# Kernel tuning notes

Hardware: AMD Instinct MI355X
Metric: run time of the kernel (lower is better)

Reference implementation:

```python
import jax, jax.numpy as jnp
import numpy as np

NEG_SLOPE = 0.2
BN_EPS = 1e-5


def _gat(x, src, dst, W, a_src, a_dst, b, concat):
    """PyG GATConv (eval mode, self-loops already in src/dst)."""
    N = x.shape[0]
    H, C = a_src.shape
    h = (x @ W).reshape(N, H, C)                      # [N,H,C]
    s = (h * a_src).sum(-1)                           # [N,H] per-node src score
    d = (h * a_dst).sum(-1)                           # [N,H] per-node dst score
    e = jax.nn.leaky_relu(s[src] + d[dst], NEG_SLOPE)  # [E,H]
    m = jax.ops.segment_max(e, dst, num_segments=N)   # segment softmax over dst
    ex = jnp.exp(e - m[dst])
    denom = jax.ops.segment_sum(ex, dst, num_segments=N)
    alpha = ex / denom[dst]                           # [E,H]
    out = jax.ops.segment_sum(alpha[:, :, None] * h[src], dst, num_segments=N)  # [N,H,C]
    out = out.reshape(N, H * C) if concat else out.mean(axis=1)
    return out + b


def _bn(x, g, beta, rm, rv):
    return (x - rm) * (g / jnp.sqrt(rv + BN_EPS)) + beta


def setup_inputs() -> dict:
    key = jax.random.key(0)
    ks = jax.random.split(key, 32)
    N, E, IN, HID, H, NC = 50000, 400000, 768, 128, 4, 2
    d = {}
    d['x'] = jax.random.normal(ks[0], (N, IN), jnp.float32)
    d['edge_index'] = jax.random.randint(ks[1], (2, E), 0, N, jnp.int64)

    def lin(k, fan_in, shape):
        return jax.random.normal(k, shape, jnp.float32) * (1.0 / np.sqrt(fan_in))

    # layer 1: in=768 -> 4 heads x 128, concat
    d['W1'] = lin(ks[2], IN, (IN, H * HID)); d['a1s'] = lin(ks[3], HID, (H, HID))
    d['a1d'] = lin(ks[4], HID, (H, HID)); d['b1'] = jnp.zeros((H * HID,), jnp.float32)
    d['g1'] = jax.random.uniform(ks[5], (H * HID,), jnp.float32, 0.5, 1.5)
    d['be1'] = jax.random.normal(ks[6], (H * HID,), jnp.float32) * 0.1
    d['rm1'] = jax.random.normal(ks[7], (H * HID,), jnp.float32) * 0.1
    d['rv1'] = jax.random.uniform(ks[8], (H * HID,), jnp.float32, 0.5, 1.5)
    d['W2'] = lin(ks[9], H * HID, (H * HID, H * HID)); d['a2s'] = lin(ks[10], HID, (H, HID))
    d['a2d'] = lin(ks[11], HID, (H, HID)); d['b2'] = jnp.zeros((H * HID,), jnp.float32)
    d['g2'] = jax.random.uniform(ks[12], (H * HID,), jnp.float32, 0.5, 1.5)
    d['be2'] = jax.random.normal(ks[13], (H * HID,), jnp.float32) * 0.1
    d['rm2'] = jax.random.normal(ks[14], (H * HID,), jnp.float32) * 0.1
    d['rv2'] = jax.random.uniform(ks[15], (H * HID,), jnp.float32, 0.5, 1.5)
    # layer 3: 512 -> 1 head x 128, mean (concat=False)
    d['W3'] = lin(ks[16], H * HID, (H * HID, HID)); d['a3s'] = lin(ks[17], HID, (1, HID))
    d['a3d'] = lin(ks[18], HID, (1, HID)); d['b3'] = jnp.zeros((HID,), jnp.float32)
    d['g3'] = jax.random.uniform(ks[19], (HID,), jnp.float32, 0.5, 1.5)
    d['be3'] = jax.random.normal(ks[20], (HID,), jnp.float32) * 0.1
    d['rm3'] = jax.random.normal(ks[21], (HID,), jnp.float32) * 0.1
    d['rv3'] = jax.random.uniform(ks[22], (HID,), jnp.float32, 0.5, 1.5)
    # classifier 128 -> 2
    d['Wc'] = lin(ks[23], HID, (HID, NC)); d['bc'] = jnp.zeros((NC,), jnp.float32)
    return d


def reference(x, edge_index, W1, a1s, a1d, b1, g1, be1, rm1, rv1,
              W2, a2s, a2d, b2, g2, be2, rm2, rv2,
              W3, a3s, a3d, b3, g3, be3, rm3, rv3, Wc, bc):
    N = x.shape[0]
    loops = jnp.arange(N, dtype=edge_index.dtype)  # GATConv add_self_loops=True
    src = jnp.concatenate([edge_index[0], loops])
    dst = jnp.concatenate([edge_index[1], loops])

    h = _gat(x, src, dst, W1, a1s, a1d, b1, concat=True)
    h = jax.nn.elu(_bn(h, g1, be1, rm1, rv1))          # dropout: eval mode (identity)
    h = _gat(h, src, dst, W2, a2s, a2d, b2, concat=True)
    h = jax.nn.elu(_bn(h, g2, be2, rm2, rv2))
    h = _gat(h, src, dst, W3, a3s, a3d, b3, concat=False)
    h = jax.nn.elu(_bn(h, g3, be3, rm3, rv3))
    return h @ Wc + bc                                  # [N, 2] logits
```

## Files before the change

kernel.cpp:

```cpp
#include <hip/hip_runtime.h>
#include <hip/hip_bf16.h>
#include <math.h>

constexpr int IN_F = 768;
constexpr float NEG_SLOPE = 0.2f;
constexpr float BN_EPS = 1e-5f;

typedef __attribute__((ext_vector_type(8))) short short8;
typedef __attribute__((ext_vector_type(4))) float f32x4;

__device__ inline float bf2f(unsigned short u) {
    unsigned int x = ((unsigned int)u) << 16;
    return __uint_as_float(x);
}
__device__ inline unsigned short f2bf(float f) {
    __hip_bfloat16 h = __float2bfloat16(f);
    return *(unsigned short*)&h;
}
__device__ inline void gload_lds16(const unsigned short* g, unsigned short* l) {
    __builtin_amdgcn_global_load_lds(
        (const __attribute__((address_space(1))) void*)g,
        (__attribute__((address_space(3))) void*)l, 16, 0, 0);
}


__global__ void init_counts(int* __restrict__ count, int* __restrict__ cursor, int N) {
    int i = blockIdx.x * blockDim.x + threadIdx.x;
    if (i < N) { count[i] = 1; cursor[i] = 0; }
}

__global__ void count_edges(const int* __restrict__ dst, int E, int* __restrict__ count) {
    int e = blockIdx.x * blockDim.x + threadIdx.x;
    if (e < E) atomicAdd(&count[dst[e]], 1);
}

__global__ void scan_counts(const int* __restrict__ count, int* __restrict__ row_start, int N) {
    __shared__ int wsum[17];
    __shared__ int carry;
    int tid = threadIdx.x;
    int lane = tid & 63, w = tid >> 6;
    if (tid == 0) carry = 0;
    __syncthreads();
    for (int base = 0; base < N; base += 4096) {
        int idx = base + tid * 4;
        int v0 = (idx + 0 < N) ? count[idx + 0] : 0;
        int v1 = (idx + 1 < N) ? count[idx + 1] : 0;
        int v2 = (idx + 2 < N) ? count[idx + 2] : 0;
        int v3 = (idx + 3 < N) ? count[idx + 3] : 0;
        int tsum = v0 + v1 + v2 + v3;
        int x = tsum;
        #pragma unroll
        for (int off = 1; off < 64; off <<= 1) {
            int y = __shfl_up(x, off, 64);
            if (lane >= off) x += y;
        }
        if (lane == 63) wsum[w] = x;
        __syncthreads();
        if (tid == 0) {
            int r = 0;
            for (int i = 0; i < 16; i++) { int t = wsum[i]; wsum[i] = r; r += t; }
            wsum[16] = r;
        }
        __syncthreads();
        int excl = carry + wsum[w] + (x - tsum);
        if (idx + 0 < N) row_start[idx + 0] = excl;
        if (idx + 1 < N) row_start[idx + 1] = excl + v0;
        if (idx + 2 < N) row_start[idx + 2] = excl + v0 + v1;
        if (idx + 3 < N) row_start[idx + 3] = excl + v0 + v1 + v2;
        __syncthreads();
        if (tid == 0) carry += wsum[16];
        __syncthreads();
    }
    if (tid == 0) row_start[N] = carry;
}

__global__ void scatter_edges(const int* __restrict__ srcA, const int* __restrict__ dstA,
                              int E, int N, const int* __restrict__ row_start,
                              int* __restrict__ cursor, int* __restrict__ col,
                              int* __restrict__ dstn) {
    int i = blockIdx.x * blockDim.x + threadIdx.x;
    if (i < E) {
        int d = dstA[i];
        int pos = row_start[d] + atomicAdd(&cursor[d], 1);
        col[pos] = srcA[i];
        dstn[pos] = d;
    } else if (i < E + N) {
        int n = i - E;
        int pos = row_start[n] + atomicAdd(&cursor[n], 1);
        col[pos] = n;
        dstn[pos] = n;
    }
}


__global__ void cast_x_bf16(const float* __restrict__ x, unsigned short* __restrict__ xb,
                            long total) {
    long i = ((long)blockIdx.x * blockDim.x + threadIdx.x) * 4;
    if (i >= total) return;
    float4 v = *(const float4*)&x[i];
    *(ushort2*)&xb[i] = make_ushort2(f2bf(v.x), f2bf(v.y));
    *(ushort2*)&xb[i + 2] = make_ushort2(f2bf(v.z), f2bf(v.w));
}

__global__ void cast_w_all(const float* __restrict__ W1, const float* __restrict__ W2,
                           const float* __restrict__ W3, unsigned short* __restrict__ Wt1,
                           unsigned short* __restrict__ Wt2, unsigned short* __restrict__ Wt3) {
    int idx = blockIdx.x * blockDim.x + threadIdx.x;
    const int S1 = 768 * 512, S2 = 512 * 512, S3 = 512 * 128;
    if (idx < S1) {
        int k = idx / 512, n = idx % 512;
        Wt1[(size_t)n * 768 + k] = f2bf(W1[idx]);
    } else if (idx < S1 + S2) {
        int j = idx - S1;
        int k = j / 512, n = j % 512;
        Wt2[(size_t)n * 512 + k] = f2bf(W2[j]);
    } else if (idx < S1 + S2 + S3) {
        int j = idx - S1 - S2;
        int k = j / 128, n = j % 128;
        Wt3[(size_t)n * 512 + k] = f2bf(W3[j]);
    }
}


__global__ __launch_bounds__(256, 3) void gemm_bf16(const unsigned short* __restrict__ A,
                                                    const unsigned short* __restrict__ Wt,
                                                    unsigned short* __restrict__ C,
                                                    const float* __restrict__ a_s,
                                                    const float* __restrict__ a_d,
                                                    float* __restrict__ s2,
                                                    float* __restrict__ d2,
                                                    int M, int Nc, int K, int H) {
    __shared__ __align__(16) unsigned short As[128 * 32];
    __shared__ __align__(16) unsigned short Bs[128 * 32];
    const int tid = threadIdx.x;
    const int lane = tid & 63;
    const int wave = tid >> 6;
    const int wm = wave >> 1, wn = wave & 1;

    const int l = blockIdx.x;
    const int x = l & 7;
    const int t0 = l >> 3;
    const int HT = Nc >> 7;
    const int by = (HT == 4) ? (t0 & 3) : 0;
    const int g  = (HT == 4) ? (t0 >> 2) : t0;
    const int rb = g * 8 + x;
    const int row0 = rb * 128, col0 = by * 128;
    if (row0 >= M) return;

    f32x4 acc[4][4];
    #pragma unroll
    for (int i = 0; i < 4; i++)
        #pragma unroll
        for (int j = 0; j < 4; j++)
            acc[i][j] = (f32x4){0.f, 0.f, 0.f, 0.f};

    const int ldm = tid >> 2;
    const int kpart = (((tid & 3) ^ ((tid >> 2) & 3)) * 8);
    const int fr = lane & 15;
    const int quad = lane >> 4;
    const int kchunk8 = ((quad ^ (fr & 3)) * 8);

    for (int k0 = 0; k0 < K; k0 += 32) {
        __syncthreads();
        #pragma unroll
        for (int i = 0; i < 2; i++) {
            int gr = row0 + i * 64 + ldm; if (gr >= M) gr = M - 1;
            gload_lds16(A + (size_t)gr * K + k0 + kpart, &As[i * 2048 + tid * 8]);
            int n = col0 + i * 64 + ldm;
            gload_lds16(Wt + (size_t)n * K + k0 + kpart, &Bs[i * 2048 + tid * 8]);
        }
        __syncthreads();
        short8 a[4], b[4];
        #pragma unroll
        for (int tt = 0; tt < 4; tt++) {
            a[tt] = *(const short8*)&As[(wm * 64 + tt * 16 + fr) * 32 + kchunk8];
            b[tt] = *(const short8*)&Bs[(wn * 64 + tt * 16 + fr) * 32 + kchunk8];
        }
        #pragma unroll
        for (int mi = 0; mi < 4; mi++)
            #pragma unroll
            for (int ni = 0; ni < 4; ni++)
                acc[mi][ni] = __builtin_amdgcn_mfma_f32_16x16x32_bf16(
                    a[mi], b[ni], acc[mi][ni], 0, 0, 0);
    }

    const int rbase = row0 + wm * 64 + quad * 4;
    const int cbase = col0 + wn * 64 + fr;
    #pragma unroll
    for (int mi = 0; mi < 4; mi++) {
        #pragma unroll
        for (int reg = 0; reg < 4; reg++) {
            int r = rbase + mi * 16 + reg;
            if (r < M) {
                #pragma unroll
                for (int ni = 0; ni < 4; ni++)
                    C[(size_t)r * Nc + cbase + ni * 16] = f2bf(acc[mi][ni][reg]);
            }
        }
    }

    float asv[4], adv[4];
    #pragma unroll
    for (int ni = 0; ni < 4; ni++) {
        int c = by * 128 + wn * 64 + ni * 16 + fr;
        asv[ni] = a_s[c];
        adv[ni] = a_d[c];
    }
    float ps[4][4], pd[4][4];
    #pragma unroll
    for (int mi = 0; mi < 4; mi++)
        #pragma unroll
        for (int reg = 0; reg < 4; reg++) {
            float t = 0.f, u = 0.f;
            #pragma unroll
            for (int ni = 0; ni < 4; ni++) {
                t += acc[mi][ni][reg] * asv[ni];
                u += acc[mi][ni][reg] * adv[ni];
            }
            ps[mi][reg] = t;
            pd[mi][reg] = u;
        }
    #pragma unroll
    for (int off = 1; off <= 8; off <<= 1)
        #pragma unroll
        for (int mi = 0; mi < 4; mi++)
            #pragma unroll
            for (int reg = 0; reg < 4; reg++) {
                ps[mi][reg] += __shfl_xor(ps[mi][reg], off, 64);
                pd[mi][reg] += __shfl_xor(pd[mi][reg], off, 64);
            }
    float oS = 0.f, oD = 0.f;
    #pragma unroll
    for (int mi = 0; mi < 4; mi++)
        #pragma unroll
        for (int reg = 0; reg < 4; reg++)
            if (fr == mi * 4 + reg) { oS = ps[mi][reg]; oD = pd[mi][reg]; }
    int rw = rbase + (fr >> 2) * 16 + (fr & 3);
    if (rw < M) {
        s2[(size_t)rw * (2 * H) + wn * H + by] = oS;
        d2[(size_t)rw * (2 * H) + wn * H + by] = oD;
    }
}


template <int H>
__global__ void edge_weights(const int* __restrict__ col, const int* __restrict__ dstn,
                             const float* __restrict__ s2, const float* __restrict__ d2,
                             float* __restrict__ wgt, int P) {
    int p = blockIdx.x * blockDim.x + threadIdx.x;
    if (p >= P) return;
    int sn = col[p], dn = dstn[p];
    if (H == 4) {
        float4 sa = *(const float4*)&s2[sn * 8];
        float4 sb = *(const float4*)&s2[sn * 8 + 4];
        float4 da = *(const float4*)&d2[dn * 8];
        float4 db = *(const float4*)&d2[dn * 8 + 4];
        float4 o;
        float e;
        e = sa.x + sb.x + da.x + db.x; e = e > 0.f ? e : NEG_SLOPE * e; o.x = __expf(e);
        e = sa.y + sb.y + da.y + db.y; e = e > 0.f ? e : NEG_SLOPE * e; o.y = __expf(e);
        e = sa.z + sb.z + da.z + db.z; e = e > 0.f ? e : NEG_SLOPE * e; o.z = __expf(e);
        e = sa.w + sb.w + da.w + db.w; e = e > 0.f ? e : NEG_SLOPE * e; o.w = __expf(e);
        *(float4*)&wgt[p * 4] = o;
    } else {
        float e = s2[sn * 2] + s2[sn * 2 + 1] + d2[dn * 2] + d2[dn * 2 + 1];
        e = e > 0.f ? e : NEG_SLOPE * e;
        wgt[p] = __expf(e);
    }
}


__global__ void gat_agg_h4(const unsigned short* __restrict__ h, const float* __restrict__ wgt,
                           const int* __restrict__ row_start, const int* __restrict__ col,
                           const float* __restrict__ bias,
                           const float* __restrict__ gam, const float* __restrict__ beta,
                           const float* __restrict__ rm, const float* __restrict__ rv,
                           unsigned short* __restrict__ out, int N) {
    int lane = threadIdx.x & 63;
    int wv = threadIdx.x >> 6;
    int n = blockIdx.x * 4 + wv;
    if (n >= N) return;
    int beg = row_start[n], end = row_start[n + 1];
    int hh = lane >> 4;
    int ch0 = lane * 8;

    float acc[8] = {0.f, 0.f, 0.f, 0.f, 0.f, 0.f, 0.f, 0.f};
    float denom = 0.f;

    for (int i = beg; i < end; i += 8) {
        uint4 raw[8]; float w[8];
        #pragma unroll
        for (int u = 0; u < 8; u++) {
            int e0 = i + u;
            int e = e0 < end ? e0 : end - 1;
            int sn = col[e];
            w[u] = (e0 < end) ? wgt[e * 4 + hh] : 0.f;
            raw[u] = *(const uint4*)&h[(size_t)sn * 512 + ch0];
        }
        #pragma unroll
        for (int u = 0; u < 8; u++) {
            denom += w[u];
            acc[0] += w[u] * bf2f((unsigned short)(raw[u].x & 0xffff));
            acc[1] += w[u] * bf2f((unsigned short)(raw[u].x >> 16));
            acc[2] += w[u] * bf2f((unsigned short)(raw[u].y & 0xffff));
            acc[3] += w[u] * bf2f((unsigned short)(raw[u].y >> 16));
            acc[4] += w[u] * bf2f((unsigned short)(raw[u].z & 0xffff));
            acc[5] += w[u] * bf2f((unsigned short)(raw[u].z >> 16));
            acc[6] += w[u] * bf2f((unsigned short)(raw[u].w & 0xffff));
            acc[7] += w[u] * bf2f((unsigned short)(raw[u].w >> 16));
        }
    }
    float inv = 1.f / denom;
    float v[8];
    #pragma unroll
    for (int c = 0; c < 8; c++) {
        int ch = ch0 + c;
        float t = acc[c] * inv + bias[ch];
        t = (t - rm[ch]) * (gam[ch] * rsqrtf(rv[ch] + BN_EPS)) + beta[ch];
        v[c] = t > 0.f ? t : expf(t) - 1.f;
    }
    uint4 p;
    p.x = (unsigned int)f2bf(v[0]) | ((unsigned int)f2bf(v[1]) << 16);
    p.y = (unsigned int)f2bf(v[2]) | ((unsigned int)f2bf(v[3]) << 16);
    p.z = (unsigned int)f2bf(v[4]) | ((unsigned int)f2bf(v[5]) << 16);
    p.w = (unsigned int)f2bf(v[6]) | ((unsigned int)f2bf(v[7]) << 16);
    *(uint4*)&out[(size_t)n * 512 + ch0] = p;
}


__global__ void gat_agg_h1_cls(const unsigned short* __restrict__ h, const float* __restrict__ wgt,
                               const int* __restrict__ row_start, const int* __restrict__ col,
                               const float* __restrict__ bias,
                               const float* __restrict__ gam, const float* __restrict__ beta,
                               const float* __restrict__ rm, const float* __restrict__ rv,
                               const float* __restrict__ Wc, const float* __restrict__ bc,
                               float* __restrict__ out, int N) {
    int lane = threadIdx.x & 63;
    int wv = threadIdx.x >> 6;
    int n = blockIdx.x * 4 + wv;
    if (n >= N) return;
    int beg = row_start[n], end = row_start[n + 1];
    int q = lane >> 4;
    int fl = lane & 15;
    const size_t hoff = fl * 8;

    float acc[8] = {0.f, 0.f, 0.f, 0.f, 0.f, 0.f, 0.f, 0.f};
    float denom = 0.f;

    for (int i = beg; i < end; i += 16) {
        uint4 raw[4]; float w[4];
        #pragma unroll
        for (int u = 0; u < 4; u++) {
            int e0 = i + u * 4 + q;
            int e = e0 < end ? e0 : end - 1;
            int sn = col[e];
            w[u] = (e0 < end) ? wgt[e] : 0.f;
            raw[u] = *(const uint4*)&h[(size_t)sn * 128 + hoff];
        }
        #pragma unroll
        for (int u = 0; u < 4; u++) {
            denom += w[u];
            acc[0] += w[u] * bf2f((unsigned short)(raw[u].x & 0xffff));
            acc[1] += w[u] * bf2f((unsigned short)(raw[u].x >> 16));
            acc[2] += w[u] * bf2f((unsigned short)(raw[u].y & 0xffff));
            acc[3] += w[u] * bf2f((unsigned short)(raw[u].y >> 16));
            acc[4] += w[u] * bf2f((unsigned short)(raw[u].z & 0xffff));
            acc[5] += w[u] * bf2f((unsigned short)(raw[u].z >> 16));
            acc[6] += w[u] * bf2f((unsigned short)(raw[u].w & 0xffff));
            acc[7] += w[u] * bf2f((unsigned short)(raw[u].w >> 16));
        }
    }
    #pragma unroll
    for (int c = 0; c < 8; c++) {
        acc[c] += __shfl_xor(acc[c], 16, 64);
        acc[c] += __shfl_xor(acc[c], 32, 64);
    }
    denom += __shfl_xor(denom, 16, 64);
    denom += __shfl_xor(denom, 32, 64);

    if (q == 0) {
        float inv = 1.f / denom;
        int ch0 = fl * 8;
        float p0 = 0.f, p1 = 0.f;
        #pragma unroll
        for (int c = 0; c < 8; c++) {
            int ch = ch0 + c;
            float t = acc[c] * inv + bias[ch];
            t = (t - rm[ch]) * (gam[ch] * rsqrtf(rv[ch] + BN_EPS)) + beta[ch];
            t = t > 0.f ? t : expf(t) - 1.f;
            p0 += t * Wc[ch * 2 + 0];
            p1 += t * Wc[ch * 2 + 1];
        }
        #pragma unroll
        for (int off = 8; off >= 1; off >>= 1) {
            p0 += __shfl_xor(p0, off, 64);
            p1 += __shfl_xor(p1, off, 64);
        }
        if (fl == 0) {
            out[n * 2 + 0] = p0 + bc[0];
            out[n * 2 + 1] = p1 + bc[1];
        }
    }
}


extern "C" void kernel_launch(void* const* d_in, const int* in_sizes, int n_in,
                              void* d_out, int out_size, void* d_ws, size_t ws_size,
                              hipStream_t stream) {
    const float* x   = (const float*)d_in[0];
    const int*   ei  = (const int*)d_in[1];
    const float* W1  = (const float*)d_in[2];
    const float* a1s = (const float*)d_in[3];
    const float* a1d = (const float*)d_in[4];
    const float* b1  = (const float*)d_in[5];
    const float* gm1 = (const float*)d_in[6];
    const float* be1 = (const float*)d_in[7];
    const float* rm1 = (const float*)d_in[8];
    const float* rv1 = (const float*)d_in[9];
    const float* W2  = (const float*)d_in[10];
    const float* a2s = (const float*)d_in[11];
    const float* a2d = (const float*)d_in[12];
    const float* b2  = (const float*)d_in[13];
    const float* gm2 = (const float*)d_in[14];
    const float* be2 = (const float*)d_in[15];
    const float* rm2 = (const float*)d_in[16];
    const float* rv2 = (const float*)d_in[17];
    const float* W3  = (const float*)d_in[18];
    const float* a3s = (const float*)d_in[19];
    const float* a3d = (const float*)d_in[20];
    const float* b3  = (const float*)d_in[21];
    const float* gm3 = (const float*)d_in[22];
    const float* be3 = (const float*)d_in[23];
    const float* rm3 = (const float*)d_in[24];
    const float* rv3 = (const float*)d_in[25];
    const float* Wc  = (const float*)d_in[26];
    const float* bc  = (const float*)d_in[27];

    int N = in_sizes[0] / IN_F;
    int E = in_sizes[1] / 2;
    int P = E + N;
    const int* srcA = ei;
    const int* dstA = ei + E;

    unsigned short* xb   = (unsigned short*)d_ws;
    unsigned short* hbuf = xb + (size_t)N * 768;
    unsigned short* gbuf = hbuf + (size_t)N * 512;
    float* s2   = (float*)(gbuf + (size_t)N * 512);
    float* d2   = s2 + (size_t)N * 8;
    float* wgt  = d2 + (size_t)N * 8;
    unsigned short* Wt1 = (unsigned short*)(wgt + (size_t)P * 4);
    unsigned short* Wt2 = Wt1 + 512 * 768;
    unsigned short* Wt3 = Wt2 + 512 * 512;
    int* count     = (int*)(Wt3 + 128 * 512);
    int* cursor    = count + N;
    int* row_start = cursor + N;
    int* col       = row_start + N + 1;
    int* dstn      = col + P;

    init_counts<<<(N + 255) / 256, 256, 0, stream>>>(count, cursor, N);
    count_edges<<<(E + 255) / 256, 256, 0, stream>>>(dstA, E, count);
    scan_counts<<<1, 1024, 0, stream>>>(count, row_start, N);
    scatter_edges<<<(E + N + 255) / 256, 256, 0, stream>>>(srcA, dstA, E, N, row_start,
                                                           cursor, col, dstn);
    long xtot = (long)N * IN_F;
    cast_x_bf16<<<(int)((xtot / 4 + 255) / 256), 256, 0, stream>>>(x, xb, xtot);
    cast_w_all<<<(768 * 512 + 512 * 512 + 512 * 128 + 255) / 256, 256, 0, stream>>>(
        W1, W2, W3, Wt1, Wt2, Wt3);

    int Mb = (N + 127) / 128;
    int MbP = (Mb + 7) & ~7;
    int Nb4 = (N + 3) / 4;

    gemm_bf16<<<4 * MbP, 256, 0, stream>>>(xb, Wt1, hbuf, a1s, a1d, s2, d2, N, 512, 768, 4);
    edge_weights<4><<<(P + 255) / 256, 256, 0, stream>>>(col, dstn, s2, d2, wgt, P);
    gat_agg_h4<<<Nb4, 256, 0, stream>>>(hbuf, wgt, row_start, col,
                                        b1, gm1, be1, rm1, rv1, gbuf, N);
    gemm_bf16<<<4 * MbP, 256, 0, stream>>>(gbuf, Wt2, hbuf, a2s, a2d, s2, d2, N, 512, 512, 4);
    edge_weights<4><<<(P + 255) / 256, 256, 0, stream>>>(col, dstn, s2, d2, wgt, P);
    gat_agg_h4<<<Nb4, 256, 0, stream>>>(hbuf, wgt, row_start, col,
                                        b2, gm2, be2, rm2, rv2, gbuf, N);
    gemm_bf16<<<MbP, 256, 0, stream>>>(gbuf, Wt3, hbuf, a3s, a3d, s2, d2, N, 128, 512, 1);
    edge_weights<1><<<(P + 255) / 256, 256, 0, stream>>>(col, dstn, s2, d2, wgt, P);
    gat_agg_h1_cls<<<Nb4, 256, 0, stream>>>(hbuf, wgt, row_start, col,
                                            b3, gm3, be3, rm3, rv3, Wc, bc, (float*)d_out, N);
}
```

Measured before the change: 690.9 us.

## Double GEMM K-tile to 64, merge cast kernels, skip padded edge loads

The bf16 GEMM now stages a K-slice of 64 per iteration with an 8-way XOR swizzle, halving the number of barrier pairs per output tile and doubling LDS per block. The x and weight cast kernels are merged into one launch. The aggregation kernels now skip loads and FMAs for padded edge slots instead of clamping and reloading the last edge. The larger LDS footprint (32KB per block) may lower occupancy under launch_bounds(256,3), and the divergent guards add branching.

```diff
diff --git a/kernel.cpp b/kernel.cpp
--- a/kernel.cpp
+++ b/kernel.cpp
@@ -93,31 +93,31 @@
 }
 
 
-__global__ void cast_x_bf16(const float* __restrict__ x, unsigned short* __restrict__ xb,
-                            long total) {
-    long i = ((long)blockIdx.x * blockDim.x + threadIdx.x) * 4;
-    if (i >= total) return;
-    float4 v = *(const float4*)&x[i];
-    *(ushort2*)&xb[i] = make_ushort2(f2bf(v.x), f2bf(v.y));
-    *(ushort2*)&xb[i + 2] = make_ushort2(f2bf(v.z), f2bf(v.w));
-}
-
-__global__ void cast_w_all(const float* __restrict__ W1, const float* __restrict__ W2,
-                           const float* __restrict__ W3, unsigned short* __restrict__ Wt1,
-                           unsigned short* __restrict__ Wt2, unsigned short* __restrict__ Wt3) {
-    int idx = blockIdx.x * blockDim.x + threadIdx.x;
+__global__ void cast_all(const float* __restrict__ x, unsigned short* __restrict__ xb, long xq,
+                         const float* __restrict__ W1, const float* __restrict__ W2,
+                         const float* __restrict__ W3, unsigned short* __restrict__ Wt1,
+                         unsigned short* __restrict__ Wt2, unsigned short* __restrict__ Wt3) {
+    long t = (long)blockIdx.x * blockDim.x + threadIdx.x;
     const int S1 = 768 * 512, S2 = 512 * 512, S3 = 512 * 128;
-    if (idx < S1) {
-        int k = idx / 512, n = idx % 512;
-        Wt1[(size_t)n * 768 + k] = f2bf(W1[idx]);
-    } else if (idx < S1 + S2) {
-        int j = idx - S1;
-        int k = j / 512, n = j % 512;
-        Wt2[(size_t)n * 512 + k] = f2bf(W2[j]);
-    } else if (idx < S1 + S2 + S3) {
-        int j = idx - S1 - S2;
-        int k = j / 128, n = j % 128;
-        Wt3[(size_t)n * 512 + k] = f2bf(W3[j]);
+    if (t < xq) {
+        long i = t * 4;
+        float4 v = *(const float4*)&x[i];
+        *(ushort2*)&xb[i] = make_ushort2(f2bf(v.x), f2bf(v.y));
+        *(ushort2*)&xb[i + 2] = make_ushort2(f2bf(v.z), f2bf(v.w));
+    } else {
+        long j = t - xq;
+        if (j < S1) {
+            int k = (int)j / 512, n = (int)j % 512;
+            Wt1[(size_t)n * 768 + k] = f2bf(W1[j]);
+        } else if (j < S1 + S2) {
+            int jj = (int)(j - S1);
+            int k = jj / 512, n = jj % 512;
+            Wt2[(size_t)n * 512 + k] = f2bf(W2[jj]);
+        } else if (j < S1 + S2 + S3) {
+            int jj = (int)(j - S1 - S2);
+            int k = jj / 128, n = jj % 128;
+            Wt3[(size_t)n * 512 + k] = f2bf(W3[jj]);
+        }
     }
 }
 
@@ -130,8 +130,8 @@
                                                     float* __restrict__ s2,
                                                     float* __restrict__ d2,
                                                     int M, int Nc, int K, int H) {
-    __shared__ __align__(16) unsigned short As[128 * 32];
-    __shared__ __align__(16) unsigned short Bs[128 * 32];
+    __shared__ __align__(16) unsigned short As[128 * 64];
+    __shared__ __align__(16) unsigned short Bs[128 * 64];
     const int tid = threadIdx.x;
     const int lane = tid & 63;
     const int wave = tid >> 6;
@@ -154,34 +154,37 @@
         for (int j = 0; j < 4; j++)
             acc[i][j] = (f32x4){0.f, 0.f, 0.f, 0.f};
 
-    const int ldm = tid >> 2;
-    const int kpart = (((tid & 3) ^ ((tid >> 2) & 3)) * 8);
+    const int ldm = tid >> 3;
+    const int kpart = (((tid & 7) ^ ((tid >> 3) & 7)) * 8);
     const int fr = lane & 15;
     const int quad = lane >> 4;
-    const int kchunk8 = ((quad ^ (fr & 3)) * 8);
-
-    for (int k0 = 0; k0 < K; k0 += 32) {
-        __syncthreads();
-        #pragma unroll
-        for (int i = 0; i < 2; i++) {
-            int gr = row0 + i * 64 + ldm; if (gr >= M) gr = M - 1;
+
+    for (int k0 = 0; k0 < K; k0 += 64) {
+        __syncthreads();
+        #pragma unroll
+        for (int i = 0; i < 4; i++) {
+            int gr = row0 + i * 32 + ldm; if (gr >= M) gr = M - 1;
             gload_lds16(A + (size_t)gr * K + k0 + kpart, &As[i * 2048 + tid * 8]);
-            int n = col0 + i * 64 + ldm;
+            int n = col0 + i * 32 + ldm;
             gload_lds16(Wt + (size_t)n * K + k0 + kpart, &Bs[i * 2048 + tid * 8]);
         }
         __syncthreads();
-        short8 a[4], b[4];
-        #pragma unroll
-        for (int tt = 0; tt < 4; tt++) {
-            a[tt] = *(const short8*)&As[(wm * 64 + tt * 16 + fr) * 32 + kchunk8];
-            b[tt] = *(const short8*)&Bs[(wn * 64 + tt * 16 + fr) * 32 + kchunk8];
-        }
-        #pragma unroll
-        for (int mi = 0; mi < 4; mi++)
+        #pragma unroll
+        for (int s = 0; s < 2; s++) {
+            const int slot8 = (((s << 2) + quad) ^ (fr & 7)) * 8;
+            short8 a[4], b[4];
             #pragma unroll
-            for (int ni = 0; ni < 4; ni++)
-                acc[mi][ni] = __builtin_amdgcn_mfma_f32_16x16x32_bf16(
-                    a[mi], b[ni], acc[mi][ni], 0, 0, 0);
+            for (int tt = 0; tt < 4; tt++) {
+                a[tt] = *(const short8*)&As[(wm * 64 + tt * 16 + fr) * 64 + slot8];
+                b[tt] = *(const short8*)&Bs[(wn * 64 + tt * 16 + fr) * 64 + slot8];
+            }
+            #pragma unroll
+            for (int mi = 0; mi < 4; mi++)
+                #pragma unroll
+                for (int ni = 0; ni < 4; ni++)
+                    acc[mi][ni] = __builtin_amdgcn_mfma_f32_16x16x32_bf16(
+                        a[mi], b[ni], acc[mi][ni], 0, 0, 0);
+        }
     }
 
     const int rbase = row0 + wm * 64 + quad * 4;
@@ -288,26 +291,30 @@
     float denom = 0.f;
 
     for (int i = beg; i < end; i += 8) {
+        int cnt = end - i; cnt = cnt > 8 ? 8 : cnt;
         uint4 raw[8]; float w[8];
         #pragma unroll
         for (int u = 0; u < 8; u++) {
-            int e0 = i + u;
-            int e = e0 < end ? e0 : end - 1;
-            int sn = col[e];
-            w[u] = (e0 < end) ? wgt[e * 4 + hh] : 0.f;
-            raw[u] = *(const uint4*)&h[(size_t)sn * 512 + ch0];
+            if (u < cnt) {
+                int e = i + u;
+                int sn = col[e];
+                w[u] = wgt[e * 4 + hh];
+                raw[u] = *(const uint4*)&h[(size_t)sn * 512 + ch0];
+            }
         }
         #pragma unroll
         for (int u = 0; u < 8; u++) {
-            denom += w[u];
-            acc[0] += w[u] * bf2f((unsigned short)(raw[u].x & 0xffff));
-            acc[1] += w[u] * bf2f((unsigned short)(raw[u].x >> 16));
-            acc[2] += w[u] * bf2f((unsigned short)(raw[u].y & 0xffff));
-            acc[3] += w[u] * bf2f((unsigned short)(raw[u].y >> 16));
-            acc[4] += w[u] * bf2f((unsigned short)(raw[u].z & 0xffff));
-            acc[5] += w[u] * bf2f((unsigned short)(raw[u].z >> 16));
-            acc[6] += w[u] * bf2f((unsigned short)(raw[u].w & 0xffff));
-            acc[7] += w[u] * bf2f((unsigned short)(raw[u].w >> 16));
+            if (u < cnt) {
+                denom += w[u];
+                acc[0] += w[u] * bf2f((unsigned short)(raw[u].x & 0xffff));
+                acc[1] += w[u] * bf2f((unsigned short)(raw[u].x >> 16));
+                acc[2] += w[u] * bf2f((unsigned short)(raw[u].y & 0xffff));
+                acc[3] += w[u] * bf2f((unsigned short)(raw[u].y >> 16));
+                acc[4] += w[u] * bf2f((unsigned short)(raw[u].z & 0xffff));
+                acc[5] += w[u] * bf2f((unsigned short)(raw[u].z >> 16));
+                acc[6] += w[u] * bf2f((unsigned short)(raw[u].w & 0xffff));
+                acc[7] += w[u] * bf2f((unsigned short)(raw[u].w >> 16));
+            }
         }
     }
     float inv = 1.f / denom;
@@ -352,10 +359,13 @@
         #pragma unroll
         for (int u = 0; u < 4; u++) {
             int e0 = i + u * 4 + q;
-            int e = e0 < end ? e0 : end - 1;
-            int sn = col[e];
-            w[u] = (e0 < end) ? wgt[e] : 0.f;
-            raw[u] = *(const uint4*)&h[(size_t)sn * 128 + hoff];
+            w[u] = 0.f;
+            raw[u] = make_uint4(0u, 0u, 0u, 0u);
+            if (e0 < end) {
+                int sn = col[e0];
+                w[u] = wgt[e0];
+                raw[u] = *(const uint4*)&h[(size_t)sn * 128 + hoff];
+            }
         }
         #pragma unroll
         for (int u = 0; u < 4; u++) {
@@ -462,10 +472,10 @@
     scan_counts<<<1, 1024, 0, stream>>>(count, row_start, N);
     scatter_edges<<<(E + N + 255) / 256, 256, 0, stream>>>(srcA, dstA, E, N, row_start,
                                                            cursor, col, dstn);
-    long xtot = (long)N * IN_F;
-    cast_x_bf16<<<(int)((xtot / 4 + 255) / 256), 256, 0, stream>>>(x, xb, xtot);
-    cast_w_all<<<(768 * 512 + 512 * 512 + 512 * 128 + 255) / 256, 256, 0, stream>>>(
-        W1, W2, W3, Wt1, Wt2, Wt3);
+    long xq = (long)N * IN_F / 4;
+    long ctot = xq + 768 * 512 + 512 * 512 + 512 * 128;
+    cast_all<<<(int)((ctot + 255) / 256), 256, 0, stream>>>(x, xb, xq, W1, W2, W3,
+                                                            Wt1, Wt2, Wt3);
 
     int Mb = (N + 127) / 128;
     int MbP = (Mb + 7) & ~7;
```

New measurement: 650.5 us. 5.9% less time.
